# Performance work log

Hardware: AMD Instinct MI355X
Metric: run time of the kernel (lower is better)

The kernel has to match this reference:

```python
import jax, jax.numpy as jnp
import numpy as np

N_RAYS = 8192
M = 524288
GX, GY, GZ = 160, 160, 128
NFEAT = 12
POS_PE, VIEW_PE = 10, 4
WIDTH = 128
POS_DIM = 3 + 3 * POS_PE * 2      # 63
VIEW_DIM = 3 + 3 * VIEW_PE * 2    # 27
DIM0 = NFEAT + POS_DIM            # 75
ACT_SHIFT = float(np.log(1.0 / (1.0 - 1e-6) - 1.0))  # density bias shift from alpha_init
INTERVAL = 0.5                    # stepsize * voxel_size_ratio
XYZ_MIN, XYZ_MAX = -1.0, 1.0


def posemb(x, n_pe):
    # x: [N,3] -> [N, 3 + 3*n_pe*2], matching cat([x, sin(x*freq), cos(x*freq)])
    freq = 2.0 ** jnp.arange(n_pe, dtype=x.dtype)
    xf = (x[..., None] * freq).reshape(x.shape[0], -1)
    return jnp.concatenate([x, jnp.sin(xf), jnp.cos(xf)], axis=-1)


def trilinear(grid, xyz):
    # grid: [X,Y,Z,C]; xyz: [M,3] in world coords. align_corners=True bilinear (grid_sample).
    sz_f = jnp.array(grid.shape[:3], jnp.float32)
    sz_i = jnp.array(grid.shape[:3], jnp.int32)
    t = (xyz - XYZ_MIN) / (XYZ_MAX - XYZ_MIN) * (sz_f - 1.0)
    t = jnp.clip(t, 0.0, sz_f - 1.0)
    i0 = jnp.clip(jnp.floor(t).astype(jnp.int32), 0, sz_i - 2)
    f = t - i0.astype(t.dtype)
    out = jnp.zeros((xyz.shape[0], grid.shape[-1]), t.dtype)
    for dx in (0, 1):
        for dy in (0, 1):
            for dz in (0, 1):
                w = ((f[:, 0] if dx else 1.0 - f[:, 0])
                     * (f[:, 1] if dy else 1.0 - f[:, 1])
                     * (f[:, 2] if dz else 1.0 - f[:, 2]))
                out = out + w[:, None] * grid[i0[:, 0] + dx, i0[:, 1] + dy, i0[:, 2] + dz]
    return out


def mask_lookup(mask, xyz):
    # nearest-neighbor maskcache_lookup: ijk = round(xyz*scale + shift)
    sz_f = jnp.array(mask.shape, jnp.float32)
    scale = (sz_f - 1.0) / (XYZ_MAX - XYZ_MIN)
    shift = -XYZ_MIN * scale
    ijk = jnp.clip(jnp.round(xyz * scale + shift).astype(jnp.int32), 0,
                   jnp.array(mask.shape, jnp.int32) - 1)
    return mask[ijk[:, 0], ijk[:, 1], ijk[:, 2]]


def alphas2weights(alpha, ray_id, n_rays):
    # segmented T_i = prod_{j<i in ray}(1-alpha_j); weights = T*alpha (ray_id sorted)
    log1a = jnp.log(jnp.clip(1.0 - alpha, 1e-10, 1.0))
    excl = jnp.cumsum(log1a) - log1a                      # global exclusive cumsum
    seg_tot = jax.ops.segment_sum(log1a, ray_id, num_segments=n_rays)
    seg_start = jnp.cumsum(seg_tot) - seg_tot             # exclusive prefix over rays
    T = jnp.exp(excl - seg_start[ray_id])
    weights = T * alpha
    alphainv_last = jnp.exp(seg_tot)
    return weights, alphainv_last


def setup_inputs() -> dict:
    key = jax.random.key(0)
    ks = jax.random.split(key, 16)
    xyz = jax.random.uniform(ks[0], (M, 3), jnp.float32) * (XYZ_MAX - XYZ_MIN) + XYZ_MIN
    ray_id = jnp.sort(jax.random.randint(ks[1], (M,), 0, N_RAYS))
    viewdirs = jax.random.normal(ks[2], (N_RAYS, 3), jnp.float32)
    viewdirs = viewdirs / jnp.linalg.norm(viewdirs, axis=-1, keepdims=True)
    mask = jax.random.uniform(ks[3], (GX, GY, GZ)) > 0.1
    density = jax.random.normal(ks[4], (GX, GY, GZ), jnp.float32) * 0.5
    k0 = jax.random.normal(ks[5], (GX, GY, GZ, NFEAT), jnp.float32) * 0.1
    s = 0.05
    W0 = jax.random.normal(ks[6], (DIM0, WIDTH), jnp.float32) * s
    b0 = jnp.zeros((WIDTH,), jnp.float32)
    W1 = jax.random.normal(ks[7], (WIDTH, WIDTH), jnp.float32) * s
    b1 = jnp.zeros((WIDTH,), jnp.float32)
    W2 = jax.random.normal(ks[8], (WIDTH, WIDTH), jnp.float32) * s
    b2 = jnp.zeros((WIDTH,), jnp.float32)
    Wr = jax.random.normal(ks[9], (WIDTH + VIEW_DIM, 3), jnp.float32) * s
    br = jnp.zeros((3,), jnp.float32)
    return {"xyz": xyz, "ray_id": ray_id, "viewdirs": viewdirs, "mask": mask,
            "density": density, "k0": k0, "W0": W0, "b0": b0, "W1": W1, "b1": b1,
            "W2": W2, "b2": b2, "Wr": Wr, "br": br}


def reference(xyz, ray_id, viewdirs, mask, density, k0, W0, b0, W1, b1, W2, b2, Wr, br):
    # 1) empty-space skipping via mask cache (kept as multiplicative mask for static shapes)
    m = mask_lookup(mask, xyz).astype(xyz.dtype)
    # 2) trilinear density query + raw2alpha
    d = trilinear(density[..., None], xyz)[:, 0]
    alpha = 1.0 - (1.0 + jnp.exp(d + ACT_SHIFT)) ** (-INTERVAL)
    alpha = alpha * m
    # 3) segmented alpha compositing (Alphas2Weights)
    weights, alphainv_last = alphas2weights(alpha, ray_id, N_RAYS)
    # 4) feature query + view MLP -> rgb
    feat = trilinear(k0, xyz)                              # [M, NFEAT]
    h = jnp.concatenate([feat, posemb(xyz, POS_PE)], -1)   # [M, DIM0]
    h = jax.nn.relu(h @ W0 + b0)
    h = jax.nn.relu(h @ W1 + b1)
    h = jax.nn.relu(h @ W2 + b2)
    ve = posemb(viewdirs, VIEW_PE)[ray_id]                 # [M, VIEW_DIM]
    rgb = jax.nn.sigmoid(jnp.concatenate([h, ve], -1) @ Wr + br)
    # 5) composite per ray + white background
    rgb_marched = jax.ops.segment_sum(weights[:, None] * rgb, ray_id, num_segments=N_RAYS)
    rgb_marched = rgb_marched + alphainv_last[:, None] * 1.0
    return rgb_marched
```

## Files before the change

kernel.cpp:

```cpp
#include <hip/hip_runtime.h>
#include <hip/hip_bf16.h>

#define M_SAMPLES 524288
#define NRAYS 8192
#define GXD 160
#define GYD 160
#define GZD 128
#define GYZ (GYD*GZD)
#define NVOX (GXD*GYD*GZD)
#define ACT_SHIFT -13.81550955796f
#define ROWA 136
#define ROWB 168
#define SAMP 128

typedef __bf16 bf16x8 __attribute__((ext_vector_type(8)));
typedef float f32x4 __attribute__((ext_vector_type(4)));
typedef float f32x16 __attribute__((ext_vector_type(16)));
typedef float f32v2 __attribute__((ext_vector_type(2)));

static __device__ inline unsigned short f2bf(float f){
  __hip_bfloat16 h = __float2bfloat16(f);
  unsigned short u; __builtin_memcpy(&u, &h, 2); return u;
}
static __device__ inline float flo(unsigned int u){ return __uint_as_float(u << 16); }
static __device__ inline float fhi(unsigned int u){ return __uint_as_float(u & 0xffff0000u); }

#if defined(__has_builtin)
#if __has_builtin(__builtin_amdgcn_cvt_pk_bf16_f32)
#define HAVE_PK_BF16 1
#endif
#if __has_builtin(__builtin_amdgcn_cvt_pk_f32_fp8) && __has_builtin(__builtin_amdgcn_cvt_pk_fp8_f32)
#define HAVE_FP8 1
#endif
#endif

static __device__ inline unsigned int packbf(float a, float b){
#ifdef HAVE_PK_BF16
  typedef __bf16 bf16v2 __attribute__((ext_vector_type(2)));
  bf16v2 r = __builtin_amdgcn_cvt_pk_bf16_f32(a, b);
  unsigned int u; __builtin_memcpy(&u, &r, 4); return u;
#else
  return (unsigned int)f2bf(a) | ((unsigned int)f2bf(b) << 16);
#endif
}

struct Tri {
  int ix, iy, iz;
  float wx0, wx1, wy0, wy1, wz0, wz1;
};
static __device__ inline Tri tri_setup(float x, float y, float z){
  Tri t;
  float tx = (x+1.f)*0.5f*(float)(GXD-1); tx = fminf(fmaxf(tx,0.f),(float)(GXD-1));
  float ty = (y+1.f)*0.5f*(float)(GYD-1); ty = fminf(fmaxf(ty,0.f),(float)(GYD-1));
  float tz = (z+1.f)*0.5f*(float)(GZD-1); tz = fminf(fmaxf(tz,0.f),(float)(GZD-1));
  t.ix = min((int)tx, GXD-2); t.iy = min((int)ty, GYD-2); t.iz = min((int)tz, GZD-2);
  float fx = tx-t.ix, fy = ty-t.iy, fz = tz-t.iz;
  t.wx0 = 1.f-fx; t.wx1 = fx; t.wy0 = 1.f-fy; t.wy1 = fy; t.wz0 = 1.f-fz; t.wz1 = fz;
  return t;
}

#define NB_REPACK (NVOX/256)
#define NB_W      186
#define NB_VE     864
__global__ __launch_bounds__(256) void k_prep(
    const float* __restrict__ density, const float* __restrict__ k0,
    uint4* __restrict__ packed,
    const unsigned int* __restrict__ mw, int* __restrict__ flag,
    const float* __restrict__ W0, const float* __restrict__ W1,
    const float* __restrict__ W2, const float* __restrict__ Wr,
    unsigned short* __restrict__ wt0, unsigned short* __restrict__ wt1,
    unsigned short* __restrict__ wt2, unsigned short* __restrict__ wtr,
    const float* __restrict__ vd, float* __restrict__ ve)
{
  int b = blockIdx.x;
  if(b < NB_REPACK){
    int v = b*256 + threadIdx.x;
    const float4* kp = (const float4*)(k0 + (size_t)v*12);
    float4 a = kp[0], bb = kp[1], c = kp[2];
#ifdef HAVE_FP8
    uint4 o;
    o.x = __float_as_uint(density[v]);
    int w;
    w = __builtin_amdgcn_cvt_pk_fp8_f32(a.x, a.y, 0, false);
    w = __builtin_amdgcn_cvt_pk_fp8_f32(a.z, a.w, w, true);
    o.y = (unsigned int)w;
    w = __builtin_amdgcn_cvt_pk_fp8_f32(bb.x, bb.y, 0, false);
    w = __builtin_amdgcn_cvt_pk_fp8_f32(bb.z, bb.w, w, true);
    o.z = (unsigned int)w;
    w = __builtin_amdgcn_cvt_pk_fp8_f32(c.x, c.y, 0, false);
    w = __builtin_amdgcn_cvt_pk_fp8_f32(c.z, c.w, w, true);
    o.w = (unsigned int)w;
    packed[v] = o;
#else
    uint4 o0, o1;
    o0.x = __float_as_uint(density[v]);
    o0.y = packbf(a.x, a.y); o0.z = packbf(a.z, a.w); o0.w = packbf(bb.x, bb.y);
    o1.x = packbf(bb.z, bb.w); o1.y = packbf(c.x, c.y); o1.z = packbf(c.z, c.w);
    o1.w = 0;
    packed[(size_t)v*2]   = o0;
    packed[(size_t)v*2+1] = o1;
#endif
    return;
  }
  if(b == NB_REPACK){
    unsigned int v = mw[threadIdx.x & 63];
    unsigned long long any = __ballot(v > 1u);
    if(threadIdx.x == 0) *flag = (any != 0ull) ? 1 : 0;
    return;
  }
  if(b < NB_REPACK + 1 + NB_W){
    int t = (b - NB_REPACK - 1)*256 + threadIdx.x;
    if(t < 128*96){
      int n = t/96, k = t%96;
      wt0[t] = f2bf((k < 75) ? W0[k*128 + n] : 0.f);
    } else if(t < 128*96 + 16384){
      int j = t - 128*96; int n = j/128, k = j%128;
      wt1[j] = f2bf(W1[k*128 + n]);
    } else if(t < 128*96 + 32768){
      int j = t - 128*96 - 16384; int n = j/128, k = j%128;
      wt2[j] = f2bf(W2[k*128 + n]);
    } else if(t < 128*96 + 32768 + 16*160){
      int j = t - 128*96 - 32768; int n = j/160, k = j%160;
      wtr[j] = f2bf((n < 3 && k < 155) ? Wr[k*3 + n] : 0.f);
    }
    return;
  }
  int t = (b - NB_REPACK - 1 - NB_W)*256 + threadIdx.x;
  if(t >= NRAYS*27) return;
  int ray = t/27, c = t%27;
  float v;
  if(c < 3) v = vd[ray*3 + c];
  else if(c < 15){
    int q = c - 3; int ci = q/4, p = q%4;
    v = sinf(vd[ray*3 + ci] * (float)(1 << p));
  } else {
    int q = c - 15; int ci = q/4, p = q%4;
    v = cosf(vd[ray*3 + ci] * (float)(1 << p));
  }
  ve[t] = v;
}

template<int KDIM, int SROW, int DROW>
static __device__ inline void layer32(const unsigned short* src, unsigned short* dst,
    const unsigned short* __restrict__ wt, const float* __restrict__ bias,
    int wave, int ln, int kh)
{
  constexpr int NS = KDIM/16;
  int tile_n = wave >> 1;
  int m0 = (wave & 1) * 2;
  const unsigned short* wbase = wt + (tile_n*32 + ln)*KDIM + kh*8;
  const unsigned short* abase0 = src + ((m0  )*32 + ln)*SROW + kh*8;
  const unsigned short* abase1 = src + ((m0+1)*32 + ln)*SROW + kh*8;
  f32x16 acc0 = {0.f,0.f,0.f,0.f,0.f,0.f,0.f,0.f,0.f,0.f,0.f,0.f,0.f,0.f,0.f,0.f};
  f32x16 acc1 = acc0;
  #pragma unroll
  for(int st = 0; st < NS; ++st){
    bf16x8 wf = *(const bf16x8*)(wbase + st*16);
    bf16x8 a0 = *(const bf16x8*)(abase0 + st*16);
    bf16x8 a1 = *(const bf16x8*)(abase1 + st*16);
    acc0 = __builtin_amdgcn_mfma_f32_32x32x16_bf16(wf, a0, acc0, 0, 0, 0);
    acc1 = __builtin_amdgcn_mfma_f32_32x32x16_bf16(wf, a1, acc1, 0, 0, 0);
  }
  #pragma unroll
  for(int rep = 0; rep < 2; ++rep){
    const f32x16& acc = rep ? acc1 : acc0;
    int scol = (m0 + rep)*32 + ln;
    #pragma unroll
    for(int g = 0; g < 4; ++g){
      int n0 = tile_n*32 + g*8 + kh*4;
      float4 bv = *(const float4*)(bias + n0);
      unsigned int lo = packbf(fmaxf(acc[4*g+0] + bv.x, 0.f), fmaxf(acc[4*g+1] + bv.y, 0.f));
      unsigned int hi = packbf(fmaxf(acc[4*g+2] + bv.z, 0.f), fmaxf(acc[4*g+3] + bv.w, 0.f));
      unsigned long long o = (unsigned long long)lo | ((unsigned long long)hi << 32);
      *(unsigned long long*)(dst + scol*DROW + n0) = o;
    }
  }
}

template<int PACKED>
__global__ __launch_bounds__(512) void k_mlp(const float* __restrict__ xyz,
    const uint4* __restrict__ packed,
    const float* __restrict__ density, const float* __restrict__ k0,
    const void* __restrict__ mask, const int* __restrict__ flag,
    const int* __restrict__ ray_id,
    const unsigned short* __restrict__ wt0, const unsigned short* __restrict__ wt1,
    const unsigned short* __restrict__ wt2, const unsigned short* __restrict__ wtr,
    const float* __restrict__ b0, const float* __restrict__ b1,
    const float* __restrict__ b2, const float* __restrict__ br,
    const float* __restrict__ ve, float4* __restrict__ rgba_out)
{
  __shared__ alignas(16) unsigned short hA[SAMP*ROWA];
  __shared__ alignas(16) unsigned short hB[SAMP*ROWB];
  __shared__ float red[SAMP][4];

  int tid = threadIdx.x;
  int lane = tid & 63, wave = tid >> 6;
  int blk = blockIdx.x*SAMP;

  {
    int smp = tid >> 2, corner = tid & 3;
    int i = blk + smp;
    float x = xyz[3*i+0], y = xyz[3*i+1], z = xyz[3*i+2];
    Tri t = tri_setup(x, y, z);
    int dx = corner & 1, dy = corner >> 1;
    float wxy = (dx ? t.wx1 : t.wx0) * (dy ? t.wy1 : t.wy0);
    float w0 = wxy*t.wz0, w1 = wxy*t.wz1;
    size_t vox = (size_t)((t.ix+dx)*GYZ + (t.iy+dy)*GZD + t.iz);
    float pd;
    float pf[12];
#ifdef HAVE_FP8
    if(PACKED){
      uint4 q0 = packed[vox], q1 = packed[vox+1];
      pd = w0*__uint_as_float(q0.x) + w1*__uint_as_float(q1.x);
      f32v2 a, b;
      a = __builtin_amdgcn_cvt_pk_f32_fp8((int)q0.y, false);
      b = __builtin_amdgcn_cvt_pk_f32_fp8((int)q1.y, false);
      pf[0] = w0*a.x + w1*b.x;  pf[1] = w0*a.y + w1*b.y;
      a = __builtin_amdgcn_cvt_pk_f32_fp8((int)q0.y, true);
      b = __builtin_amdgcn_cvt_pk_f32_fp8((int)q1.y, true);
      pf[2] = w0*a.x + w1*b.x;  pf[3] = w0*a.y + w1*b.y;
      a = __builtin_amdgcn_cvt_pk_f32_fp8((int)q0.z, false);
      b = __builtin_amdgcn_cvt_pk_f32_fp8((int)q1.z, false);
      pf[4] = w0*a.x + w1*b.x;  pf[5] = w0*a.y + w1*b.y;
      a = __builtin_amdgcn_cvt_pk_f32_fp8((int)q0.z, true);
      b = __builtin_amdgcn_cvt_pk_f32_fp8((int)q1.z, true);
      pf[6] = w0*a.x + w1*b.x;  pf[7] = w0*a.y + w1*b.y;
      a = __builtin_amdgcn_cvt_pk_f32_fp8((int)q0.w, false);
      b = __builtin_amdgcn_cvt_pk_f32_fp8((int)q1.w, false);
      pf[8] = w0*a.x + w1*b.x;  pf[9] = w0*a.y + w1*b.y;
      a = __builtin_amdgcn_cvt_pk_f32_fp8((int)q0.w, true);
      b = __builtin_amdgcn_cvt_pk_f32_fp8((int)q1.w, true);
      pf[10]= w0*a.x + w1*b.x;  pf[11]= w0*a.y + w1*b.y;
    }
#else
    if(PACKED){
      const uint4* pv = packed + vox*2;
      uint4 q0 = pv[0], q1 = pv[1], q2 = pv[2], q3 = pv[3];
      pd = w0*__uint_as_float(q0.x) + w1*__uint_as_float(q2.x);
      pf[0]  = w0*flo(q0.y) + w1*flo(q2.y);  pf[1]  = w0*fhi(q0.y) + w1*fhi(q2.y);
      pf[2]  = w0*flo(q0.z) + w1*flo(q2.z);  pf[3]  = w0*fhi(q0.z) + w1*fhi(q2.z);
      pf[4]  = w0*flo(q0.w) + w1*flo(q2.w);  pf[5]  = w0*fhi(q0.w) + w1*fhi(q2.w);
      pf[6]  = w0*flo(q1.x) + w1*flo(q3.x);  pf[7]  = w0*fhi(q1.x) + w1*fhi(q3.x);
      pf[8]  = w0*flo(q1.y) + w1*flo(q3.y);  pf[9]  = w0*fhi(q1.y) + w1*fhi(q3.y);
      pf[10] = w0*flo(q1.z) + w1*flo(q3.z);  pf[11] = w0*fhi(q1.z) + w1*fhi(q3.z);
    }
#endif
    if(!PACKED){
      pd = w0*density[vox] + w1*density[vox+1];
      const float4* v = (const float4*)(k0 + vox*12);
      float4 a0 = v[0], a1 = v[1], a2 = v[2];
      float4 c0 = v[3], c1 = v[4], c2 = v[5];
      pf[0] = w0*a0.x + w1*c0.x;  pf[1] = w0*a0.y + w1*c0.y;
      pf[2] = w0*a0.z + w1*c0.z;  pf[3] = w0*a0.w + w1*c0.w;
      pf[4] = w0*a1.x + w1*c1.x;  pf[5] = w0*a1.y + w1*c1.y;
      pf[6] = w0*a1.z + w1*c1.z;  pf[7] = w0*a1.w + w1*c1.w;
      pf[8] = w0*a2.x + w1*c2.x;  pf[9] = w0*a2.y + w1*c2.y;
      pf[10]= w0*a2.z + w1*c2.z;  pf[11]= w0*a2.w + w1*c2.w;
    }
    #pragma unroll
    for(int m2 = 1; m2 < 4; m2 <<= 1){
      pd += __shfl_xor(pd, m2);
      #pragma unroll
      for(int j = 0; j < 12; ++j) pf[j] += __shfl_xor(pf[j], m2);
    }
    if(corner == 0){
      int mx = (int)rintf(x*79.5f + 79.5f); mx = min(max(mx,0), GXD-1);
      int my = (int)rintf(y*79.5f + 79.5f); my = min(max(my,0), GYD-1);
      int mz = (int)rintf(z*63.5f + 63.5f); mz = min(max(mz,0), GZD-1);
      int midx = mx*GYZ + my*GZD + mz;
      bool mm = (*flag) ? (((const unsigned char*)mask)[midx] != 0)
                        : (((const int*)mask)[midx] != 0);
      float e = expf(pd + ACT_SHIFT);
      float alpha = 1.f - rsqrtf(1.f + e);
      if(!mm) alpha = 0.f;
      red[smp][3] = alpha;
      unsigned int d[8];
      #pragma unroll
      for(int j = 0; j < 6; ++j) d[j] = packbf(pf[2*j], pf[2*j+1]);
      d[6] = packbf(x, y);
      d[7] = packbf(z, __sinf(x));
      uint4* p = (uint4*)(hA + smp*ROWA);
      p[0] = make_uint4(d[0],d[1],d[2],d[3]);
      p[1] = make_uint4(d[4],d[5],d[6],d[7]);
    } else if(corner == 1){
      uint4* p = (uint4*)(hA + smp*ROWA + 80);
      p[0] = make_uint4(0,0,0,0);
      p[1] = make_uint4(0,0,0,0);
    } else {
      int ray = ray_id[i];
      int cb = (corner - 2) * 16;
      unsigned int d[8];
      #pragma unroll
      for(int j = 0; j < 8; ++j){
        int c = cb + 2*j;
        float a = (c     < 27) ? ve[ray*27 + c]     : 0.f;
        float b = (c + 1 < 27) ? ve[ray*27 + c + 1] : 0.f;
        d[j] = packbf(a, b);
      }
      uint4* p = (uint4*)(hB + smp*ROWB + 128 + cb);
      p[0] = make_uint4(d[0],d[1],d[2],d[3]);
      p[1] = make_uint4(d[4],d[5],d[6],d[7]);
    }
  }

  {
    int smp = tid & 127, chunk = 1 + (tid >> 7);
    int i2 = blk + smp;
    float x = xyz[3*i2+0], y = xyz[3*i2+1], z = xyz[3*i2+2];
    float vv[16];
    #pragma unroll
    for(int j = 0; j < 16; ++j){
      int c = chunk*16 + j;
      float r;
      if(c >= 75) r = 0.f;
      else {
        int q = (c < 45) ? (c-15) : (c-45);
        int ci = q/10, p = q - ci*10;
        float xv = (ci == 0) ? x : ((ci == 1) ? y : z);
        float a = xv * (float)(1 << p);
        r = (c < 45) ? __sinf(a) : __cosf(a);
      }
      vv[j] = r;
    }
    unsigned int d[8];
    #pragma unroll
    for(int j = 0; j < 8; ++j) d[j] = packbf(vv[2*j], vv[2*j+1]);
    uint4* p = (uint4*)(hA + smp*ROWA + chunk*16);
    p[0] = make_uint4(d[0],d[1],d[2],d[3]);
    p[1] = make_uint4(d[4],d[5],d[6],d[7]);
  }
  __syncthreads();

  int ln = lane & 31, kh = lane >> 5;
  layer32< 96, ROWA, ROWB>(hA, hB, wt0, b0, wave, ln, kh);  __syncthreads();
  layer32<128, ROWB, ROWA>(hB, hA, wt1, b1, wave, ln, kh);  __syncthreads();
  layer32<128, ROWA, ROWB>(hA, hB, wt2, b2, wave, ln, kh);  __syncthreads();

  {
    int col = lane & 15, q = lane >> 4;
    int mt = wave;
    f32x4 acc = {0.f, 0.f, 0.f, 0.f};
    const unsigned short* arow = hB + (mt*16 + col)*ROWB + q*8;
    const unsigned short* wrow = wtr + col*160 + q*8;
    #pragma unroll
    for(int ks = 0; ks < 5; ++ks){
      bf16x8 af = *(const bf16x8*)(arow + ks*32);
      bf16x8 bfr = *(const bf16x8*)(wrow + ks*32);
      acc = __builtin_amdgcn_mfma_f32_16x16x32_bf16(af, bfr, acc, 0, 0, 0);
    }
    if(col < 3){
      #pragma unroll
      for(int r = 0; r < 4; ++r){
        int sl = mt*16 + q*4 + r;
        float v = acc[r] + br[col];
        red[sl][col] = 1.f / (1.f + expf(-v));
      }
    }
  }
  __syncthreads();

  if(tid < SAMP){
    rgba_out[blk + tid] = make_float4(red[tid][0], red[tid][1], red[tid][2], red[tid][3]);
  }
}

__global__ __launch_bounds__(256) void k_comp2(const int* __restrict__ ray_id,
    const float4* __restrict__ rgba, float* __restrict__ out)
{
  int r = blockIdx.x*4 + (threadIdx.x >> 6);
  int lane = threadIdx.x & 63;
  int lo = 0, hi = M_SAMPLES;
  while(lo < hi){ int mid = (lo+hi) >> 1; if(ray_id[mid] < r) lo = mid+1; else hi = mid; }
  int s = lo;
  int lo2 = s, hi2 = M_SAMPLES;
  while(lo2 < hi2){ int mid = (lo2+hi2) >> 1; if(ray_id[mid] < r+1) lo2 = mid+1; else hi2 = mid; }
  int e = lo2;

  float carry = 1.f;
  float ar = 0.f, ag = 0.f, ab = 0.f;
  for(int base = s; base < e; base += 64){
    int idx = base + lane;
    float4 c = (idx < e) ? rgba[idx] : make_float4(0.f,0.f,0.f,0.f);
    float a = c.w;
    float incl = 1.f - a;
    #pragma unroll
    for(int d2 = 1; d2 < 64; d2 <<= 1){
      float t = __shfl_up(incl, d2);
      if(lane >= d2) incl *= t;
    }
    float excl = __shfl_up(incl, 1);
    if(lane == 0) excl = 1.f;
    float w = carry * excl * a;
    ar += w*c.x; ag += w*c.y; ab += w*c.z;
    carry *= __shfl(incl, 63);
  }
  #pragma unroll
  for(int m2 = 1; m2 < 64; m2 <<= 1){
    ar += __shfl_xor(ar, m2);
    ag += __shfl_xor(ag, m2);
    ab += __shfl_xor(ab, m2);
  }
  if(lane == 0){
    out[3*r+0] = ar + carry;
    out[3*r+1] = ag + carry;
    out[3*r+2] = ab + carry;
  }
}

extern "C" void kernel_launch(void* const* d_in, const int* in_sizes, int n_in,
                              void* d_out, int out_size, void* d_ws, size_t ws_size,
                              hipStream_t stream)
{
  const float* xyz      = (const float*)d_in[0];
  const int*   ray_id   = (const int*)  d_in[1];
  const float* viewdirs = (const float*)d_in[2];
  const void*  mask     =               d_in[3];
  const float* density  = (const float*)d_in[4];
  const float* k0       = (const float*)d_in[5];
  const float* W0 = (const float*)d_in[6];  const float* b0 = (const float*)d_in[7];
  const float* W1 = (const float*)d_in[8];  const float* b1 = (const float*)d_in[9];
  const float* W2 = (const float*)d_in[10]; const float* b2 = (const float*)d_in[11];
  const float* Wr = (const float*)d_in[12]; const float* br = (const float*)d_in[13];
  float* out = (float*)d_out;

  char* ws = (char*)d_ws;
  size_t off = 0;
  auto take = [&](size_t nbytes) -> void* {
    void* p = ws + off;
    off = (off + nbytes + 255) & ~(size_t)255;
    return p;
  };
  int*            flag    = (int*)           take(4);
  unsigned short* wt0     = (unsigned short*)take(128*96*2);
  unsigned short* wt1     = (unsigned short*)take(128*128*2);
  unsigned short* wt2     = (unsigned short*)take(128*128*2);
  unsigned short* wtr     = (unsigned short*)take(16*160*2);
  float*          ve      = (float*)         take((size_t)NRAYS*27*4);
  float4*         rgba_ws = (float4*)        take((size_t)M_SAMPLES*16);
#ifdef HAVE_FP8
  uint4*          packed  = (uint4*)         take((size_t)NVOX*16);
#else
  uint4*          packed  = (uint4*)         take((size_t)NVOX*32);
#endif
  bool use_packed = (ws_size >= off);

  k_prep<<<NB_REPACK + 1 + NB_W + NB_VE, 256, 0, stream>>>(
      density, k0, packed, (const unsigned int*)mask, flag,
      W0, W1, W2, Wr, wt0, wt1, wt2, wtr, viewdirs, ve);
  if(use_packed){
    k_mlp<1><<<M_SAMPLES/SAMP, 512, 0, stream>>>(xyz, packed, density, k0, mask, flag,
                                                 ray_id, wt0, wt1, wt2, wtr,
                                                 b0, b1, b2, br, ve, rgba_ws);
  } else {
    k_mlp<0><<<M_SAMPLES/SAMP, 512, 0, stream>>>(xyz, packed, density, k0, mask, flag,
                                                 ray_id, wt0, wt1, wt2, wtr,
                                                 b0, b1, b2, br, ve, rgba_ws);
  }
  k_comp2<<<NRAYS/4, 256, 0, stream>>>(ray_id, rgba_ws, out);
}
```

Baseline: 434.9 us.

## Precompute per-ray view-embedding contribution to rgb logits instead of per-sample GEMM

The view-direction embedding is constant per ray, so its product with the last 27 rows of Wr plus the bias is computed once per ray in the prep kernel in fp32. The MLP kernel then runs the rgb head over only the 128 hidden columns (4 MFMA steps instead of 5) and adds the per-ray term looked up via ray_id. This removes the per-sample gather of 27 view features, the hB staging row extension (ROWB shrinks to 136), and shrinks shared memory. It also switches to fast __sinf/__cosf for the view embedding, which slightly changes precision.

```diff
diff --git a/kernel.cpp b/kernel.cpp
--- a/kernel.cpp
+++ b/kernel.cpp
@@ -10,7 +10,7 @@
 #define NVOX (GXD*GYD*GZD)
 #define ACT_SHIFT -13.81550955796f
 #define ROWA 136
-#define ROWB 168
+#define ROWB 136
 #define SAMP 128
 
 typedef __bf16 bf16x8 __attribute__((ext_vector_type(8)));
@@ -60,17 +60,18 @@
 }
 
 #define NB_REPACK (NVOX/256)
-#define NB_W      186
-#define NB_VE     864
+#define NB_W      184
+#define NB_RT     (NRAYS/256)
 __global__ __launch_bounds__(256) void k_prep(
     const float* __restrict__ density, const float* __restrict__ k0,
     uint4* __restrict__ packed,
     const unsigned int* __restrict__ mw, int* __restrict__ flag,
     const float* __restrict__ W0, const float* __restrict__ W1,
     const float* __restrict__ W2, const float* __restrict__ Wr,
+    const float* __restrict__ br,
     unsigned short* __restrict__ wt0, unsigned short* __restrict__ wt1,
     unsigned short* __restrict__ wt2, unsigned short* __restrict__ wtr,
-    const float* __restrict__ vd, float* __restrict__ ve)
+    const float* __restrict__ vd, float* __restrict__ rayterm3)
 {
   int b = blockIdx.x;
   if(b < NB_REPACK){
@@ -119,25 +120,34 @@
     } else if(t < 128*96 + 32768){
       int j = t - 128*96 - 16384; int n = j/128, k = j%128;
       wt2[j] = f2bf(W2[k*128 + n]);
-    } else if(t < 128*96 + 32768 + 16*160){
-      int j = t - 128*96 - 32768; int n = j/160, k = j%160;
-      wtr[j] = f2bf((n < 3 && k < 155) ? Wr[k*3 + n] : 0.f);
+    } else if(t < 128*96 + 32768 + 16*128){
+      int j = t - 128*96 - 32768; int n = j/128, k = j%128;
+      wtr[j] = f2bf((n < 3) ? Wr[k*3 + n] : 0.f);
     }
     return;
   }
-  int t = (b - NB_REPACK - 1 - NB_W)*256 + threadIdx.x;
-  if(t >= NRAYS*27) return;
-  int ray = t/27, c = t%27;
-  float v;
-  if(c < 3) v = vd[ray*3 + c];
-  else if(c < 15){
-    int q = c - 3; int ci = q/4, p = q%4;
-    v = sinf(vd[ray*3 + ci] * (float)(1 << p));
-  } else {
-    int q = c - 15; int ci = q/4, p = q%4;
-    v = cosf(vd[ray*3 + ci] * (float)(1 << p));
-  }
-  ve[t] = v;
+  int ray = (b - NB_REPACK - 1 - NB_W)*256 + threadIdx.x;
+  if(ray >= NRAYS) return;
+  float v0 = vd[ray*3+0], v1 = vd[ray*3+1], v2 = vd[ray*3+2];
+  float vej[27];
+  vej[0] = v0; vej[1] = v1; vej[2] = v2;
+  #pragma unroll
+  for(int ci = 0; ci < 3; ++ci){
+    float xv = (ci == 0) ? v0 : ((ci == 1) ? v1 : v2);
+    #pragma unroll
+    for(int p = 0; p < 4; ++p){
+      float arg = xv * (float)(1 << p);
+      vej[3 + ci*4 + p]  = __sinf(arg);
+      vej[15 + ci*4 + p] = __cosf(arg);
+    }
+  }
+  float rt0 = br[0], rt1 = br[1], rt2 = br[2];
+  #pragma unroll
+  for(int j = 0; j < 27; ++j){
+    const float* wr = Wr + (128 + j)*3;
+    rt0 += vej[j]*wr[0]; rt1 += vej[j]*wr[1]; rt2 += vej[j]*wr[2];
+  }
+  rayterm3[ray*3+0] = rt0; rayterm3[ray*3+1] = rt1; rayterm3[ray*3+2] = rt2;
 }
 
 template<int KDIM, int SROW, int DROW>
@@ -186,12 +196,13 @@
     const unsigned short* __restrict__ wt0, const unsigned short* __restrict__ wt1,
     const unsigned short* __restrict__ wt2, const unsigned short* __restrict__ wtr,
     const float* __restrict__ b0, const float* __restrict__ b1,
-    const float* __restrict__ b2, const float* __restrict__ br,
-    const float* __restrict__ ve, float4* __restrict__ rgba_out)
+    const float* __restrict__ b2,
+    const float* __restrict__ rayterm3, float4* __restrict__ rgba_out)
 {
   __shared__ alignas(16) unsigned short hA[SAMP*ROWA];
   __shared__ alignas(16) unsigned short hB[SAMP*ROWB];
   __shared__ float red[SAMP][4];
+  __shared__ int ray_s[SAMP];
 
   int tid = threadIdx.x;
   int lane = tid & 63, wave = tid >> 6;
@@ -286,20 +297,7 @@
       uint4* p = (uint4*)(hA + smp*ROWA + 80);
       p[0] = make_uint4(0,0,0,0);
       p[1] = make_uint4(0,0,0,0);
-    } else {
-      int ray = ray_id[i];
-      int cb = (corner - 2) * 16;
-      unsigned int d[8];
-      #pragma unroll
-      for(int j = 0; j < 8; ++j){
-        int c = cb + 2*j;
-        float a = (c     < 27) ? ve[ray*27 + c]     : 0.f;
-        float b = (c + 1 < 27) ? ve[ray*27 + c + 1] : 0.f;
-        d[j] = packbf(a, b);
-      }
-      uint4* p = (uint4*)(hB + smp*ROWB + 128 + cb);
-      p[0] = make_uint4(d[0],d[1],d[2],d[3]);
-      p[1] = make_uint4(d[4],d[5],d[6],d[7]);
+      ray_s[smp] = ray_id[i];
     }
   }
 
@@ -341,9 +339,9 @@
     int mt = wave;
     f32x4 acc = {0.f, 0.f, 0.f, 0.f};
     const unsigned short* arow = hB + (mt*16 + col)*ROWB + q*8;
-    const unsigned short* wrow = wtr + col*160 + q*8;
-    #pragma unroll
-    for(int ks = 0; ks < 5; ++ks){
+    const unsigned short* wrow = wtr + col*128 + q*8;
+    #pragma unroll
+    for(int ks = 0; ks < 4; ++ks){
       bf16x8 af = *(const bf16x8*)(arow + ks*32);
       bf16x8 bfr = *(const bf16x8*)(wrow + ks*32);
       acc = __builtin_amdgcn_mfma_f32_16x16x32_bf16(af, bfr, acc, 0, 0, 0);
@@ -352,7 +350,7 @@
       #pragma unroll
       for(int r = 0; r < 4; ++r){
         int sl = mt*16 + q*4 + r;
-        float v = acc[r] + br[col];
+        float v = acc[r] + rayterm3[ray_s[sl]*3 + col];
         red[sl][col] = 1.f / (1.f + expf(-v));
       }
     }
@@ -430,31 +428,31 @@
     off = (off + nbytes + 255) & ~(size_t)255;
     return p;
   };
-  int*            flag    = (int*)           take(4);
-  unsigned short* wt0     = (unsigned short*)take(128*96*2);
-  unsigned short* wt1     = (unsigned short*)take(128*128*2);
-  unsigned short* wt2     = (unsigned short*)take(128*128*2);
-  unsigned short* wtr     = (unsigned short*)take(16*160*2);
-  float*          ve      = (float*)         take((size_t)NRAYS*27*4);
-  float4*         rgba_ws = (float4*)        take((size_t)M_SAMPLES*16);
+  int*            flag     = (int*)           take(4);
+  unsigned short* wt0      = (unsigned short*)take(128*96*2);
+  unsigned short* wt1      = (unsigned short*)take(128*128*2);
+  unsigned short* wt2      = (unsigned short*)take(128*128*2);
+  unsigned short* wtr      = (unsigned short*)take(16*128*2);
+  float*          rayterm3 = (float*)         take((size_t)NRAYS*3*4);
+  float4*         rgba_ws  = (float4*)        take((size_t)M_SAMPLES*16);
 #ifdef HAVE_FP8
-  uint4*          packed  = (uint4*)         take((size_t)NVOX*16);
+  uint4*          packed   = (uint4*)         take((size_t)NVOX*16);
 #else
-  uint4*          packed  = (uint4*)         take((size_t)NVOX*32);
+  uint4*          packed   = (uint4*)         take((size_t)NVOX*32);
 #endif
   bool use_packed = (ws_size >= off);
 
-  k_prep<<<NB_REPACK + 1 + NB_W + NB_VE, 256, 0, stream>>>(
+  k_prep<<<NB_REPACK + 1 + NB_W + NB_RT, 256, 0, stream>>>(
       density, k0, packed, (const unsigned int*)mask, flag,
-      W0, W1, W2, Wr, wt0, wt1, wt2, wtr, viewdirs, ve);
+      W0, W1, W2, Wr, br, wt0, wt1, wt2, wtr, viewdirs, rayterm3);
   if(use_packed){
     k_mlp<1><<<M_SAMPLES/SAMP, 512, 0, stream>>>(xyz, packed, density, k0, mask, flag,
                                                  ray_id, wt0, wt1, wt2, wtr,
-                                                 b0, b1, b2, br, ve, rgba_ws);
+                                                 b0, b1, b2, rayterm3, rgba_ws);
   } else {
     k_mlp<0><<<M_SAMPLES/SAMP, 512, 0, stream>>>(xyz, packed, density, k0, mask, flag,
                                                  ray_id, wt0, wt1, wt2, wtr,
-                                                 b0, b1, b2, br, ve, rgba_ws);
+                                                 b0, b1, b2, rayterm3, rgba_ws);
   }
   k_comp2<<<NRAYS/4, 256, 0, stream>>>(ray_id, rgba_ws, out);
 }
```

After: 434.1 us. No clear change (-0.2%).
